# Performance work log

Measured on AMD Instinct MI355X. Metric: run time of the kernel, lower is better.

## Reference

```python
import jax, jax.numpy as jnp
import numpy as np

B, N, C = 8, 2048, 256
E = 32768
H, C_OUT = 8, 64
NEG_SLOPE = 0.2


def setup_inputs() -> dict:
    key = jax.random.key(0)
    k1, k2, k3, k4, k5 = jax.random.split(key, 5)
    x = jax.random.normal(k1, (B, N, C), dtype=jnp.float32)
    edge_index = jax.random.randint(k2, (2, E), 0, N, dtype=jnp.int64)
    W_lin = jax.random.normal(k3, (C, H * C_OUT), dtype=jnp.float32) * 0.05
    att_src = jax.random.normal(k4, (H, C_OUT), dtype=jnp.float32) * 0.05
    att_dst = jax.random.normal(k5, (H, C_OUT), dtype=jnp.float32) * 0.05
    bias = jnp.zeros((H * C_OUT,), dtype=jnp.float32)
    return {"x": x, "edge_index": edge_index, "W_lin": W_lin,
            "att_src": att_src, "att_dst": att_dst, "bias": bias}


def _segment_softmax(logits, segment_ids, num_segments):
    # stable softmax over edges grouped by destination node
    seg_max = jax.ops.segment_max(logits, segment_ids, num_segments=num_segments)
    logits = logits - seg_max[segment_ids]
    exp = jnp.exp(logits)
    seg_sum = jax.ops.segment_sum(exp, segment_ids, num_segments=num_segments)
    return exp / (seg_sum[segment_ids] + 1e-16)


def reference(x, edge_index, W_lin, att_src, att_dst, bias):
    Bn = B * N
    # node linear projection -> [B*N, H, C_out]
    xt = (x.reshape(Bn, C) @ W_lin).reshape(Bn, H, C_OUT)

    # batch the shared edge_index: block b offset by b*N, then append self-loops
    offs = (jnp.arange(B, dtype=edge_index.dtype) * N)[None, :, None]  # [1,B,1]
    ei = (edge_index[:, None, :] + offs).reshape(2, B * E)              # [2,B*E]
    loops = jnp.arange(Bn, dtype=edge_index.dtype)
    src = jnp.concatenate([ei[0], loops])
    dst = jnp.concatenate([ei[1], loops])

    x_j = xt[src]  # [E_tot, H, C_out] source features
    x_i = xt[dst]
    alpha = jnp.einsum('ehc,hc->eh', x_j, att_src) + jnp.einsum('ehc,hc->eh', x_i, att_dst)
    alpha = jax.nn.leaky_relu(alpha, NEG_SLOPE)
    alpha = _segment_softmax(alpha, dst, Bn)  # softmax over incoming edges per node/head

    msg = x_j * alpha[:, :, None]
    out = jax.ops.segment_sum(msg, dst, num_segments=Bn)  # [B*N, H, C_out]
    out = out.reshape(B, N, H * C_OUT) + bias
    return out
```

## Files before the change

### kernel.cpp

```cpp
#include <hip/hip_runtime.h>
#include <hip/hip_bf16.h>

#define BDIM 8
#define NNODE 2048
#define CIN 256
#define NEDGE 32768
#define NHEAD 8
#define COUT 64
#define HC 512
#define BN_TOT 16384
#define NEG_SLOPE 0.2f

typedef __hip_bfloat16 bf16;
typedef __attribute__((ext_vector_type(8))) short bfrag;
typedef __attribute__((ext_vector_type(4))) float ffrag;

static __device__ __forceinline__ short f2b(float f) {
    __hip_bfloat16 h = __float2bfloat16(f);
    return *(short*)&h;
}
static __device__ __forceinline__ float b2f(short s) {
    return __uint_as_float(((unsigned)(unsigned short)s) << 16);
}

__global__ __launch_bounds__(256) void cvt_kernel(const float* __restrict__ x,
                                                  const float* __restrict__ W,
                                                  short* __restrict__ xbf,
                                                  short* __restrict__ WT) {
    const int b = blockIdx.x;
    if (b < 128) {
        __shared__ float t[32][33];
        const int kt = b >> 4;
        const int nt = b & 15;
        const int tx = threadIdx.x & 31, ty = threadIdx.x >> 5;
#pragma unroll
        for (int i = 0; i < 4; ++i)
            t[ty + 8 * i][tx] = W[(kt * 32 + ty + 8 * i) * HC + nt * 32 + tx];
        __syncthreads();
#pragma unroll
        for (int i = 0; i < 4; ++i)
            WT[(nt * 32 + ty + 8 * i) * CIN + kt * 32 + tx] = f2b(t[tx][ty + 8 * i]);
    } else {
        const int t = (b - 128) * 256 + threadIdx.x;
        const float4* px = (const float4*)x;
        float4 v0 = px[t * 2], v1 = px[t * 2 + 1];
        bfrag o;
        o[0] = f2b(v0.x); o[1] = f2b(v0.y); o[2] = f2b(v0.z); o[3] = f2b(v0.w);
        o[4] = f2b(v1.x); o[5] = f2b(v1.y); o[6] = f2b(v1.z); o[7] = f2b(v1.w);
        *(bfrag*)&xbf[t * 8] = o;
    }
}

__global__ __launch_bounds__(256) void gemm_mfma(const short* __restrict__ xbf,
                                                 const short* __restrict__ WT,
                                                 short* __restrict__ xtb) {
    __shared__ __align__(16) short As[128][40];
    __shared__ __align__(16) short Bs[128][40];

    const int tid  = threadIdx.x;
    const int row0 = blockIdx.y * 128;
    const int col0 = blockIdx.x * 128;
    const int w    = tid >> 6;
    const int lane = tid & 63;
    const int wm   = (w & 1) * 64;
    const int wn   = (w >> 1) * 64;
    const int fm   = lane & 15;
    const int fq   = lane >> 4;

    const int sr = tid >> 2;
    const int sc = (tid & 3) * 8;

    ffrag acc[4][4] = {};

    for (int k0 = 0; k0 < CIN; k0 += 32) {
        bfrag a0 = *(const bfrag*)&xbf[(row0 + sr) * CIN + k0 + sc];
        bfrag a1 = *(const bfrag*)&xbf[(row0 + sr + 64) * CIN + k0 + sc];
        bfrag b0 = *(const bfrag*)&WT[(col0 + sr) * CIN + k0 + sc];
        bfrag b1 = *(const bfrag*)&WT[(col0 + sr + 64) * CIN + k0 + sc];
        __syncthreads();
        *(bfrag*)&As[sr][sc]      = a0;
        *(bfrag*)&As[sr + 64][sc] = a1;
        *(bfrag*)&Bs[sr][sc]      = b0;
        *(bfrag*)&Bs[sr + 64][sc] = b1;
        __syncthreads();

        bfrag af[4], bfr[4];
#pragma unroll
        for (int g = 0; g < 4; ++g) {
            af[g]  = *(const bfrag*)&As[wm + g * 16 + fm][fq * 8];
            bfr[g] = *(const bfrag*)&Bs[wn + g * 16 + fm][fq * 8];
        }
#pragma unroll
        for (int mg = 0; mg < 4; ++mg)
#pragma unroll
            for (int ng = 0; ng < 4; ++ng)
                acc[mg][ng] = __builtin_amdgcn_mfma_f32_16x16x32_bf16(
                    af[mg], bfr[ng], acc[mg][ng], 0, 0, 0);
    }

#pragma unroll
    for (int mg = 0; mg < 4; ++mg)
#pragma unroll
        for (int ng = 0; ng < 4; ++ng) {
            const int rbase = row0 + wm + mg * 16 + fq * 4;
            const int c     = col0 + wn + ng * 16 + fm;
#pragma unroll
            for (int r = 0; r < 4; ++r)
                xtb[(rbase + r) * HC + c] = f2b(acc[mg][ng][r]);
        }
}

__global__ __launch_bounds__(256) void att_scores(const short* __restrict__ xtb,
                                                  const float* __restrict__ att_src,
                                                  const float* __restrict__ att_dst,
                                                  float* __restrict__ ssrc,
                                                  float* __restrict__ sdst) {
    const int n = blockIdx.x * 4 + (threadIdx.x >> 6);
    const int l = threadIdx.x & 63;

    bfrag xv = *(const bfrag*)&xtb[n * HC + l * 8];
    const float4* as = (const float4*)&att_src[l * 8];
    float4 a0 = as[0], a1 = as[1];
    const float4* ad = (const float4*)&att_dst[l * 8];
    float4 b0 = ad[0], b1 = ad[1];

    float xf[8];
#pragma unroll
    for (int k = 0; k < 8; ++k) xf[k] = b2f(xv[k]);

    float ps = xf[0] * a0.x + xf[1] * a0.y + xf[2] * a0.z + xf[3] * a0.w +
               xf[4] * a1.x + xf[5] * a1.y + xf[6] * a1.z + xf[7] * a1.w;
    float pd = xf[0] * b0.x + xf[1] * b0.y + xf[2] * b0.z + xf[3] * b0.w +
               xf[4] * b1.x + xf[5] * b1.y + xf[6] * b1.z + xf[7] * b1.w;

    ps += __shfl_xor(ps, 4); ps += __shfl_xor(ps, 2); ps += __shfl_xor(ps, 1);
    pd += __shfl_xor(pd, 4); pd += __shfl_xor(pd, 2); pd += __shfl_xor(pd, 1);

    if ((l & 7) == 0) {
        ssrc[n * NHEAD + (l >> 3)] = ps;
        sdst[n * NHEAD + (l >> 3)] = pd;
    }
}

__global__ void count_edges(const int* __restrict__ ei, int* __restrict__ cnt) {
    int t = blockIdx.x * 256 + threadIdx.x;
    atomicAdd(&cnt[ei[NEDGE + t]], 1);
}

__global__ __launch_bounds__(256) void scan_rowptr(const int* __restrict__ cnt,
                                                   int* __restrict__ rowptr,
                                                   int* __restrict__ widx) {
    __shared__ int sums[256];
    const int t = threadIdx.x;
    int v[8];
    int tot = 0;
#pragma unroll
    for (int i = 0; i < 8; ++i) { v[i] = cnt[t * 8 + i]; tot += v[i]; }
    sums[t] = tot;
    __syncthreads();
    for (int off = 1; off < 256; off <<= 1) {
        int x = (t >= off) ? sums[t - off] : 0;
        __syncthreads();
        sums[t] += x;
        __syncthreads();
    }
    int run = sums[t] - tot;
    int base[8];
#pragma unroll
    for (int i = 0; i < 8; ++i) { base[i] = run; run += v[i]; }
#pragma unroll
    for (int b = 0; b < BDIM; ++b) {
#pragma unroll
        for (int i = 0; i < 8; ++i) {
            int n = t * 8 + i;
            int val = b * NEDGE + base[i];
            rowptr[b * NNODE + n] = val;
            widx[b * NNODE + n] = val;
        }
    }
}

__global__ void scatter_edges(const int* __restrict__ ei, int* __restrict__ widx,
                              int* __restrict__ col) {
    int t = blockIdx.x * 256 + threadIdx.x;
    int b = t >> 15;
    int e = t & (NEDGE - 1);
    int s = ei[e];
    int d = ei[NEDGE + e];
    int p = atomicAdd(&widx[b * NNODE + d], 1);
    col[p] = b * NNODE + s;
}

__global__ __launch_bounds__(256) void aggregate(const short* __restrict__ xtb,
                                                 const float* __restrict__ ssrc,
                                                 const float* __restrict__ sdst,
                                                 const int* __restrict__ cnt,
                                                 const int* __restrict__ rowptr,
                                                 const int* __restrict__ col,
                                                 const float* __restrict__ bias,
                                                 float* __restrict__ out) {
    __shared__ float wlds[4][NHEAD][68];
    const int nb   = threadIdx.x >> 6;
    const int lane = threadIdx.x & 63;
    const int blk  = blockIdx.x;
    const int i    = (blk & 7) * NNODE + (blk >> 3) * 4 + nb;
    const int n    = i & (NNODE - 1);
    const int deg  = cnt[n];
    const int start = rowptr[i];
    const int h    = lane >> 3;
    const int sub  = lane & 7;
    float* wrow = &wlds[nb][0][0];

    for (int t = lane; t < NHEAD * 68; t += 64) wrow[t] = 0.f;

    const float sdh = sdst[i * NHEAD + h];
    float selfv = ssrc[i * NHEAD + h] + sdh;
    selfv = selfv >= 0.f ? selfv : NEG_SLOPE * selfv;

    float m = selfv;
    for (int e = sub; e < deg; e += 8) {
        int j = col[start + e];
        float v = ssrc[j * NHEAD + h] + sdh;
        v = v >= 0.f ? v : NEG_SLOPE * v;
        if (e < 64) wrow[h * 68 + e] = v;
        m = fmaxf(m, v);
    }
    m = fmaxf(m, __shfl_xor(m, 4));
    m = fmaxf(m, __shfl_xor(m, 2));
    m = fmaxf(m, __shfl_xor(m, 1));

    float sp = 0.f;
    for (int e = sub; e < deg; e += 8) {
        float v;
        if (e < 64) {
            v = wrow[h * 68 + e];
        } else {
            int j = col[start + e];
            v = ssrc[j * NHEAD + h] + sdh;
            v = v >= 0.f ? v : NEG_SLOPE * v;
        }
        float w = __expf(v - m);
        if (e < 64) wrow[h * 68 + e] = w;
        sp += w;
    }
    sp += __shfl_xor(sp, 4); sp += __shfl_xor(sp, 2); sp += __shfl_xor(sp, 1);
    const float eself = __expf(selfv - m);
    const float inv = 1.f / (sp + eself + 1e-16f);

    const int c8 = lane * 8;
    float acc[8] = {};

    {
        bfrag xv = *(const bfrag*)&xtb[i * HC + c8];
#pragma unroll
        for (int k = 0; k < 8; ++k) acc[k] += eself * b2f(xv[k]);
    }

    const int degc = min(deg, 64);
    const int deg4 = (degc + 3) & ~3;
    for (int e0 = 0; e0 < deg4; e0 += 4) {
        float4 w4 = *(const float4*)&wrow[h * 68 + e0];
#pragma unroll
        for (int u = 0; u < 4; ++u) {
            int ec = min(e0 + u, deg - 1);
            int j = col[start + ec];
            bfrag xv = *(const bfrag*)&xtb[j * HC + c8];
            float wv = (&w4.x)[u];
#pragma unroll
            for (int k = 0; k < 8; ++k) acc[k] += wv * b2f(xv[k]);
        }
    }
    for (int e = 64; e < deg; ++e) {
        int j = col[start + e];
        float v = ssrc[j * NHEAD + h] + sdh;
        v = v >= 0.f ? v : NEG_SLOPE * v;
        float wv = __expf(v - m);
        bfrag xv = *(const bfrag*)&xtb[j * HC + c8];
#pragma unroll
        for (int k = 0; k < 8; ++k) acc[k] += wv * b2f(xv[k]);
    }

    const float4 b0 = *(const float4*)&bias[c8];
    const float4 b1 = *(const float4*)&bias[c8 + 4];
    float4 o0 = {acc[0] * inv + b0.x, acc[1] * inv + b0.y,
                 acc[2] * inv + b0.z, acc[3] * inv + b0.w};
    float4 o1 = {acc[4] * inv + b1.x, acc[5] * inv + b1.y,
                 acc[6] * inv + b1.z, acc[7] * inv + b1.w};
    *(float4*)&out[i * HC + c8]     = o0;
    *(float4*)&out[i * HC + c8 + 4] = o1;
}

extern "C" void kernel_launch(void* const* d_in, const int* in_sizes, int n_in,
                              void* d_out, int out_size, void* d_ws, size_t ws_size,
                              hipStream_t stream) {
    const float* x       = (const float*)d_in[0];
    const int*   ei      = (const int*)d_in[1];
    const float* W       = (const float*)d_in[2];
    const float* att_src = (const float*)d_in[3];
    const float* att_dst = (const float*)d_in[4];
    const float* bias    = (const float*)d_in[5];
    float* out = (float*)d_out;

    char* ws = (char*)d_ws;
    short* xtb    = (short*)(ws);
    float* ssrc   = (float*)(ws + 16777216);
    float* sdst   = (float*)(ws + 17301504);
    int*   cnt    = (int*)(ws + 17825792);
    int*   rowptr = (int*)(ws + 17833984);
    int*   widx   = (int*)(ws + 17899520);
    int*   col    = (int*)(ws + 17965056);
    short* xbf    = (short*)(ws + 19013632);
    short* WT     = (short*)(ws + 27402240);
    hipMemsetAsync(cnt, 0, NNODE * sizeof(int), stream);

    cvt_kernel<<<128 + 2048, 256, 0, stream>>>(x, W, xbf, WT);
    gemm_mfma<<<dim3(HC / 128, BN_TOT / 128), 256, 0, stream>>>(xbf, WT, xtb);
    att_scores<<<BN_TOT / 4, 256, 0, stream>>>(xtb, att_src, att_dst, ssrc, sdst);
    count_edges<<<NEDGE / 256, 256, 0, stream>>>(ei, cnt);
    scan_rowptr<<<1, 256, 0, stream>>>(cnt, rowptr, widx);
    scatter_edges<<<(BDIM * NEDGE) / 256, 256, 0, stream>>>(ei, widx, col);
    aggregate<<<BN_TOT / 4, 256, 0, stream>>>(xtb, ssrc, sdst, cnt, rowptr, col, bias, out);
}
```

Before: 147.0 us.

## Fuse CSR build into prep and GEMM kernels, batch gathers in aggregate

The edge-count histogram and prefix scan move into a single extra block of the conversion kernel, which uses a shared-memory histogram, so the memset and two launches disappear. The edge scatter runs as extra blocks inside the GEMM launch, and the per-batch rowptr array is replaced by a single base offset per node. The aggregate kernel caches neighbour indices in LDS and issues eight feature gathers per iteration to raise memory-level parallelism. In exchange, the one histogram block serialises 32K LDS atomics and may become the critical path of the prep launch.

```diff
diff --git a/kernel.cpp b/kernel.cpp
--- a/kernel.cpp
+++ b/kernel.cpp
@@ -23,10 +23,14 @@
     return __uint_as_float(((unsigned)(unsigned short)s) << 16);
 }
 
-__global__ __launch_bounds__(256) void cvt_kernel(const float* __restrict__ x,
-                                                  const float* __restrict__ W,
-                                                  short* __restrict__ xbf,
-                                                  short* __restrict__ WT) {
+__global__ __launch_bounds__(256) void prep_kernel(const float* __restrict__ x,
+                                                   const float* __restrict__ W,
+                                                   const int* __restrict__ ei,
+                                                   short* __restrict__ xbf,
+                                                   short* __restrict__ WT,
+                                                   int* __restrict__ cnt,
+                                                   int* __restrict__ rowptr0,
+                                                   int* __restrict__ widx) {
     const int b = blockIdx.x;
     if (b < 128) {
         __shared__ float t[32][33];
@@ -40,7 +44,7 @@
 #pragma unroll
         for (int i = 0; i < 4; ++i)
             WT[(nt * 32 + ty + 8 * i) * CIN + kt * 32 + tx] = f2b(t[tx][ty + 8 * i]);
-    } else {
+    } else if (b < 2176) {
         const int t = (b - 128) * 256 + threadIdx.x;
         const float4* px = (const float4*)x;
         float4 v0 = px[t * 2], v1 = px[t * 2 + 1];
@@ -48,18 +52,69 @@
         o[0] = f2b(v0.x); o[1] = f2b(v0.y); o[2] = f2b(v0.z); o[3] = f2b(v0.w);
         o[4] = f2b(v1.x); o[5] = f2b(v1.y); o[6] = f2b(v1.z); o[7] = f2b(v1.w);
         *(bfrag*)&xbf[t * 8] = o;
-    }
-}
-
-__global__ __launch_bounds__(256) void gemm_mfma(const short* __restrict__ xbf,
-                                                 const short* __restrict__ WT,
-                                                 short* __restrict__ xtb) {
+    } else {
+        __shared__ int hcnt[NNODE];
+        __shared__ int sums[256];
+        const int t = threadIdx.x;
+        for (int k = t; k < NNODE; k += 256) hcnt[k] = 0;
+        __syncthreads();
+        const int* dst = ei + NEDGE;
+        for (int e = t; e < NEDGE; e += 256) atomicAdd(&hcnt[dst[e]], 1);
+        __syncthreads();
+        int v[8];
+        int tot = 0;
+#pragma unroll
+        for (int i = 0; i < 8; ++i) { v[i] = hcnt[t * 8 + i]; tot += v[i]; }
+        sums[t] = tot;
+        __syncthreads();
+        for (int off = 1; off < 256; off <<= 1) {
+            int xv = (t >= off) ? sums[t - off] : 0;
+            __syncthreads();
+            sums[t] += xv;
+            __syncthreads();
+        }
+        int run = sums[t] - tot;
+        int base[8];
+#pragma unroll
+        for (int i = 0; i < 8; ++i) { base[i] = run; run += v[i]; }
+#pragma unroll
+        for (int i = 0; i < 8; ++i) {
+            const int n = t * 8 + i;
+            cnt[n] = v[i];
+            rowptr0[n] = base[i];
+        }
+#pragma unroll
+        for (int b2 = 0; b2 < BDIM; ++b2)
+#pragma unroll
+            for (int i = 0; i < 8; ++i)
+                widx[b2 * NNODE + t * 8 + i] = b2 * NEDGE + base[i];
+    }
+}
+
+__global__ __launch_bounds__(256) void gemm_scatter(const short* __restrict__ xbf,
+                                                    const short* __restrict__ WT,
+                                                    short* __restrict__ xtb,
+                                                    const int* __restrict__ ei,
+                                                    int* __restrict__ widx,
+                                                    int* __restrict__ col) {
+    const int blk = blockIdx.x;
+    if (blk >= 512) {
+        const int t = (blk - 512) * 256 + threadIdx.x;
+        const int b = t >> 15;
+        const int e = t & (NEDGE - 1);
+        const int s = ei[e];
+        const int d = ei[NEDGE + e];
+        const int p = atomicAdd(&widx[b * NNODE + d], 1);
+        col[p] = b * NNODE + s;
+        return;
+    }
+
     __shared__ __align__(16) short As[128][40];
     __shared__ __align__(16) short Bs[128][40];
 
     const int tid  = threadIdx.x;
-    const int row0 = blockIdx.y * 128;
-    const int col0 = blockIdx.x * 128;
+    const int row0 = (blk >> 2) * 128;
+    const int col0 = (blk & 3) * 128;
     const int w    = tid >> 6;
     const int lane = tid & 63;
     const int wm   = (w & 1) * 64;
@@ -142,76 +197,31 @@
     }
 }
 
-__global__ void count_edges(const int* __restrict__ ei, int* __restrict__ cnt) {
-    int t = blockIdx.x * 256 + threadIdx.x;
-    atomicAdd(&cnt[ei[NEDGE + t]], 1);
-}
-
-__global__ __launch_bounds__(256) void scan_rowptr(const int* __restrict__ cnt,
-                                                   int* __restrict__ rowptr,
-                                                   int* __restrict__ widx) {
-    __shared__ int sums[256];
-    const int t = threadIdx.x;
-    int v[8];
-    int tot = 0;
-#pragma unroll
-    for (int i = 0; i < 8; ++i) { v[i] = cnt[t * 8 + i]; tot += v[i]; }
-    sums[t] = tot;
-    __syncthreads();
-    for (int off = 1; off < 256; off <<= 1) {
-        int x = (t >= off) ? sums[t - off] : 0;
-        __syncthreads();
-        sums[t] += x;
-        __syncthreads();
-    }
-    int run = sums[t] - tot;
-    int base[8];
-#pragma unroll
-    for (int i = 0; i < 8; ++i) { base[i] = run; run += v[i]; }
-#pragma unroll
-    for (int b = 0; b < BDIM; ++b) {
-#pragma unroll
-        for (int i = 0; i < 8; ++i) {
-            int n = t * 8 + i;
-            int val = b * NEDGE + base[i];
-            rowptr[b * NNODE + n] = val;
-            widx[b * NNODE + n] = val;
-        }
-    }
-}
-
-__global__ void scatter_edges(const int* __restrict__ ei, int* __restrict__ widx,
-                              int* __restrict__ col) {
-    int t = blockIdx.x * 256 + threadIdx.x;
-    int b = t >> 15;
-    int e = t & (NEDGE - 1);
-    int s = ei[e];
-    int d = ei[NEDGE + e];
-    int p = atomicAdd(&widx[b * NNODE + d], 1);
-    col[p] = b * NNODE + s;
-}
-
 __global__ __launch_bounds__(256) void aggregate(const short* __restrict__ xtb,
                                                  const float* __restrict__ ssrc,
                                                  const float* __restrict__ sdst,
                                                  const int* __restrict__ cnt,
-                                                 const int* __restrict__ rowptr,
+                                                 const int* __restrict__ rowptr0,
                                                  const int* __restrict__ col,
                                                  const float* __restrict__ bias,
                                                  float* __restrict__ out) {
     __shared__ float wlds[4][NHEAD][68];
+    __shared__ int   jlds[4][64];
     const int nb   = threadIdx.x >> 6;
     const int lane = threadIdx.x & 63;
     const int blk  = blockIdx.x;
-    const int i    = (blk & 7) * NNODE + (blk >> 3) * 4 + nb;
+    const int bidx = blk & 7;
+    const int i    = bidx * NNODE + (blk >> 3) * 4 + nb;
     const int n    = i & (NNODE - 1);
     const int deg  = cnt[n];
-    const int start = rowptr[i];
+    const int start = bidx * NEDGE + rowptr0[n];
     const int h    = lane >> 3;
     const int sub  = lane & 7;
     float* wrow = &wlds[nb][0][0];
+    int*   jrow = &jlds[nb][0];
 
     for (int t = lane; t < NHEAD * 68; t += 64) wrow[t] = 0.f;
+    jrow[lane] = i;
 
     const float sdh = sdst[i * NHEAD + h];
     float selfv = ssrc[i * NHEAD + h] + sdh;
@@ -222,7 +232,10 @@
         int j = col[start + e];
         float v = ssrc[j * NHEAD + h] + sdh;
         v = v >= 0.f ? v : NEG_SLOPE * v;
-        if (e < 64) wrow[h * 68 + e] = v;
+        if (e < 64) {
+            wrow[h * 68 + e] = v;
+            if (h == 0) jrow[e] = j;
+        }
         m = fmaxf(m, v);
     }
     m = fmaxf(m, __shfl_xor(m, 4));
@@ -257,17 +270,26 @@
     }
 
     const int degc = min(deg, 64);
-    const int deg4 = (degc + 3) & ~3;
-    for (int e0 = 0; e0 < deg4; e0 += 4) {
-        float4 w4 = *(const float4*)&wrow[h * 68 + e0];
-#pragma unroll
-        for (int u = 0; u < 4; ++u) {
-            int ec = min(e0 + u, deg - 1);
-            int j = col[start + ec];
-            bfrag xv = *(const bfrag*)&xtb[j * HC + c8];
-            float wv = (&w4.x)[u];
-#pragma unroll
-            for (int k = 0; k < 8; ++k) acc[k] += wv * b2f(xv[k]);
+    const int degp = (degc + 7) & ~7;
+    for (int e0 = 0; e0 < degp; e0 += 8) {
+        float4 wA = *(const float4*)&wrow[h * 68 + e0];
+        float4 wB = *(const float4*)&wrow[h * 68 + e0 + 4];
+        int4 jA = *(const int4*)&jrow[e0];
+        int4 jB = *(const int4*)&jrow[e0 + 4];
+        bfrag x0 = *(const bfrag*)&xtb[jA.x * HC + c8];
+        bfrag x1 = *(const bfrag*)&xtb[jA.y * HC + c8];
+        bfrag x2 = *(const bfrag*)&xtb[jA.z * HC + c8];
+        bfrag x3 = *(const bfrag*)&xtb[jA.w * HC + c8];
+        bfrag x4 = *(const bfrag*)&xtb[jB.x * HC + c8];
+        bfrag x5 = *(const bfrag*)&xtb[jB.y * HC + c8];
+        bfrag x6 = *(const bfrag*)&xtb[jB.z * HC + c8];
+        bfrag x7 = *(const bfrag*)&xtb[jB.w * HC + c8];
+#pragma unroll
+        for (int k = 0; k < 8; ++k) {
+            acc[k] += wA.x * b2f(x0[k]) + wA.y * b2f(x1[k]) +
+                      wA.z * b2f(x2[k]) + wA.w * b2f(x3[k]) +
+                      wB.x * b2f(x4[k]) + wB.y * b2f(x5[k]) +
+                      wB.z * b2f(x6[k]) + wB.w * b2f(x7[k]);
         }
     }
     for (int e = 64; e < deg; ++e) {
@@ -302,22 +324,17 @@
     float* out = (float*)d_out;
 
     char* ws = (char*)d_ws;
-    short* xtb    = (short*)(ws);
-    float* ssrc   = (float*)(ws + 16777216);
-    float* sdst   = (float*)(ws + 17301504);
-    int*   cnt    = (int*)(ws + 17825792);
-    int*   rowptr = (int*)(ws + 17833984);
-    int*   widx   = (int*)(ws + 17899520);
-    int*   col    = (int*)(ws + 17965056);
-    short* xbf    = (short*)(ws + 19013632);
-    short* WT     = (short*)(ws + 27402240);
-    hipMemsetAsync(cnt, 0, NNODE * sizeof(int), stream);
-
-    cvt_kernel<<<128 + 2048, 256, 0, stream>>>(x, W, xbf, WT);
-    gemm_mfma<<<dim3(HC / 128, BN_TOT / 128), 256, 0, stream>>>(xbf, WT, xtb);
+    short* xtb     = (short*)(ws);
+    float* ssrc    = (float*)(ws + 16777216);
+    float* sdst    = (float*)(ws + 17301504);
+    int*   cnt     = (int*)(ws + 17825792);
+    int*   rowptr0 = (int*)(ws + 17833984);
+    int*   widx    = (int*)(ws + 17842176);
+    int*   col     = (int*)(ws + 17907712);
+    short* xbf     = (short*)(ws + 18956288);
+    short* WT      = (short*)(ws + 27344896);
+    prep_kernel<<<2177, 256, 0, stream>>>(x, W, ei, xbf, WT, cnt, rowptr0, widx);
+    gemm_scatter<<<1536, 256, 0, stream>>>(xbf, WT, xtb, ei, widx, col);
     att_scores<<<BN_TOT / 4, 256, 0, stream>>>(xtb, att_src, att_dst, ssrc, sdst);
-    count_edges<<<NEDGE / 256, 256, 0, stream>>>(ei, cnt);
-    scan_rowptr<<<1, 256, 0, stream>>>(cnt, rowptr, widx);
-    scatter_edges<<<(BDIM * NEDGE) / 256, 256, 0, stream>>>(ei, widx, col);
-    aggregate<<<BN_TOT / 4, 256, 0, stream>>>(xtb, ssrc, sdst, cnt, rowptr, col, bias, out);
-}
+    aggregate<<<BN_TOT / 4, 256, 0, stream>>>(xtb, ssrc, sdst, cnt, rowptr0, col, bias, out);
+}
```

After: 169.4 us. 15.3% more time.
